# Optimization experiments

Measured on AMD Instinct MI355X. Metric: run time of the kernel, lower is better.

## Reference

```python
import jax, jax.numpy as jnp
import numpy as np

N, K, D = 262144, 1024, 64


def setup_inputs() -> dict:
    key = jax.random.key(0)
    k1, k2 = jax.random.split(key)
    input_data = jax.random.normal(k1, (N, D), dtype=jnp.float32)
    codewords = jax.random.normal(k2, (K, D), dtype=jnp.float32)
    return {"input_data": input_data, "codewords": codewords}


def reference(input_data, codewords):
    # input_data: [N, D], codewords: [K, D]
    x = input_data.reshape(-1, codewords.shape[1])
    x2 = jnp.sum(x * x, axis=1, keepdims=True)          # [N, 1]
    c2 = jnp.sum(codewords * codewords, axis=1)          # [K]
    d2 = x2 + c2[None, :] - 2.0 * (x @ codewords.T)      # [N, K]
    distances = jnp.sqrt(jnp.maximum(d2, 0.0))
    quantized_indices = jnp.argmin(distances, axis=1)    # [N] int
    quantized_distances = jnp.take_along_axis(
        distances, quantized_indices[:, None], axis=1
    )[:, 0]                                              # [N]
    quantized_data = codewords[quantized_indices]        # [N, D]
    return (quantized_indices, quantized_distances, quantized_data)
```

## Files before the change

### kernel.cpp

```cpp
#include <hip/hip_runtime.h>


#define N_PTS 262144
#define K_CW  1024
#define DIM   64
#define CHUNK_B 36864
#define HALF_B  (4 * CHUNK_B)

typedef __attribute__((ext_vector_type(8)))  short short8;
typedef __attribute__((ext_vector_type(16))) float floatx16;

__device__ __forceinline__ unsigned short f2bf(float f) {
    unsigned u = __float_as_uint(f);
    return (unsigned short)((u + 0x7FFFu + ((u >> 16) & 1u)) >> 16);
}
__device__ __forceinline__ float bf2f(unsigned short h) {
    return __uint_as_float(((unsigned)h) << 16);
}
__device__ __forceinline__ float dot4(float4 a, float4 b) {
    return a.x*b.x + a.y*b.y + a.z*b.z + a.w*b.w;
}
__device__ __forceinline__ void async_cp16(const void* g, void* l) {
    __builtin_amdgcn_global_load_lds(
        (const __attribute__((address_space(1))) unsigned int*)g,
        (__attribute__((address_space(3))) unsigned int*)l, 16, 0, 0);
}

__global__ void vq_prep(const float* __restrict__ cw, unsigned char* __restrict__ ws) {
    const int k = blockIdx.x * 256 + threadIdx.x;
    const int ch = k >> 7, r = k & 127;
    unsigned short* chunk = (unsigned short*)(ws + (size_t)ch * CHUNK_B);
    unsigned short* hi = chunk + r * 72;
    unsigned short* lo = hi + 9216;
    const float4* cr = (const float4*)cw + (size_t)k * 16;
    float c2 = 0.f;
    #pragma unroll
    for (int j = 0; j < 16; ++j) {
        float4 v = cr[j];
        c2 += dot4(v, v);
        float4 m = make_float4(-2.f*v.x, -2.f*v.y, -2.f*v.z, -2.f*v.w);
        unsigned short h0 = f2bf(m.x), h1 = f2bf(m.y), h2 = f2bf(m.z), h3 = f2bf(m.w);
        unsigned short l0 = f2bf(m.x - bf2f(h0)), l1 = f2bf(m.y - bf2f(h1)),
                       l2 = f2bf(m.z - bf2f(h2)), l3 = f2bf(m.w - bf2f(h3));
        uint2 hv, lv;
        hv.x = (unsigned)h0 | ((unsigned)h1 << 16);
        hv.y = (unsigned)h2 | ((unsigned)h3 << 16);
        lv.x = (unsigned)l0 | ((unsigned)l1 << 16);
        lv.y = (unsigned)l2 | ((unsigned)l3 << 16);
        *(uint2*)(hi + j * 4) = hv;
        *(uint2*)(lo + j * 4) = lv;
    }
    *(float*)(hi + 64) = c2;
}

__launch_bounds__(512, 2)
__global__ void vq_main(const float* __restrict__ x,
                        const float* __restrict__ cw,
                        const unsigned char* __restrict__ ws,
                        float* __restrict__ out) {
    __shared__ __align__(16) unsigned char sB[HALF_B];

    const int tid  = threadIdx.x;
    const int w    = tid >> 6;
    const int lane = tid & 63;
    const int q    = lane >> 5;
    const int l31  = lane & 31;
    const int half  = blockIdx.x & 1;
    const int pbase = (blockIdx.x >> 1) * 512;
    const float4* __restrict__ x4  = (const float4*)x;
    const float4* __restrict__ c4p = (const float4*)cw;

    {
        const unsigned char* g = ws + (size_t)half * HALF_B + tid * 16;
        unsigned char* l = sB + tid * 16;
        #pragma unroll
        for (int s = 0; s < 18; ++s) async_cp16(g + s * 8192, l + s * 8192);
    }

    short8 ah[2][4], al[2][4];
    #pragma unroll
    for (int rt = 0; rt < 2; ++rt) {
        const int row = pbase + w * 64 + rt * 32 + l31;
        const float4* xr = x4 + (size_t)row * 16;
        #pragma unroll
        for (int ks = 0; ks < 4; ++ks) {
            float4 va = xr[ks * 4 + q * 2];
            float4 vb = xr[ks * 4 + q * 2 + 1];
            float f[8] = {va.x, va.y, va.z, va.w, vb.x, vb.y, vb.z, vb.w};
            short8 h, l;
            #pragma unroll
            for (int j = 0; j < 8; ++j) {
                unsigned short hb = f2bf(f[j]);
                h[j] = (short)hb;
                l[j] = (short)f2bf(f[j] - bf2f(hb));
            }
            ah[rt][ks] = h; al[rt][ks] = l;
        }
    }

    __syncthreads();

    const unsigned short* __restrict__ S = (const unsigned short*)sB;

    float bu[32];
    #pragma unroll
    for (int s = 0; s < 32; ++s) bu[s] = 3.4e38f;

    #pragma unroll 4
    for (int g = 0; g < 16; ++g) {
        const unsigned short* chS = S + (g >> 2) * (CHUNK_B / 2);
        const int nrow = (g & 3) * 32 + l31;
        short8 bh[4], bl[4];
        #pragma unroll
        for (int ks = 0; ks < 4; ++ks) {
            bh[ks] = *(const short8*)&chS[nrow * 72 + ks * 16 + q * 8];
            bl[ks] = *(const short8*)&chS[9216 + nrow * 72 + ks * 16 + q * 8];
        }
        const float c2v = *(const float*)&chS[nrow * 72 + 64];
        floatx16 a0, a1;
        #pragma unroll
        for (int r = 0; r < 16; ++r) { a0[r] = c2v; a1[r] = c2v; }
        __builtin_amdgcn_s_setprio(1);
        #pragma unroll
        for (int ks = 0; ks < 4; ++ks) {
            a0 = __builtin_amdgcn_mfma_f32_32x32x16_bf16(ah[0][ks], bh[ks], a0, 0, 0, 0);
            a1 = __builtin_amdgcn_mfma_f32_32x32x16_bf16(ah[1][ks], bh[ks], a1, 0, 0, 0);
            a0 = __builtin_amdgcn_mfma_f32_32x32x16_bf16(al[0][ks], bh[ks], a0, 0, 0, 0);
            a1 = __builtin_amdgcn_mfma_f32_32x32x16_bf16(al[1][ks], bh[ks], a1, 0, 0, 0);
            a0 = __builtin_amdgcn_mfma_f32_32x32x16_bf16(ah[0][ks], bl[ks], a0, 0, 0, 0);
            a1 = __builtin_amdgcn_mfma_f32_32x32x16_bf16(ah[1][ks], bl[ks], a1, 0, 0, 0);
        }
        __builtin_amdgcn_s_setprio(0);
        const unsigned tag = (unsigned)g;
        #pragma unroll
        for (int r = 0; r < 16; ++r) {
            unsigned u0 = (__float_as_uint(a0[r]) & 0xFFFFFFE0u) | tag;
            bu[r] = fminf(bu[r], __uint_as_float(u0));
            unsigned u1 = (__float_as_uint(a1[r]) & 0xFFFFFFE0u) | tag;
            bu[16 + r] = fminf(bu[16 + r], __uint_as_float(u1));
        }
    }

    int keep_i0 = 0, keep_i1 = 0;
    #pragma unroll
    for (int s = 0; s < 32; ++s) {
        const float v = bu[s];
        float m1 = v;
        #pragma unroll
        for (int m = 1; m < 32; m <<= 1) m1 = fminf(m1, __shfl_xor(m1, m));
        unsigned long long bm = __ballot(v == m1);
        const int wl = __ffs((unsigned)(bm >> (q * 32))) - 1;
        const float v2 = (l31 == wl) ? 3.4e38f : v;
        float m2 = v2;
        #pragma unroll
        for (int m = 1; m < 32; m <<= 1) m2 = fminf(m2, __shfl_xor(m2, m));
        unsigned long long bm2 = __ballot(v2 == m2);
        const int wl2 = __ffs((unsigned)(bm2 >> (q * 32))) - 1;
        const int i0 = (int)(((__float_as_uint(m1) & 31u) << 5) | (unsigned)wl);
        const int i1 = (int)(((__float_as_uint(m2) & 31u) << 5) | (unsigned)wl2);
        if (l31 == s) { keep_i0 = i0; keep_i1 = i1; }
    }

    const int rS   = l31 & 15;
    const int prow = (l31 >> 4) * 32 + (rS & 3) + 8 * (rS >> 2) + 4 * q;
    const int p    = pbase + w * 64 + prow;
    const int ia = keep_i0, ib = keep_i1;
    const float4* xr = x4 + (size_t)p * 16;
    const float4* ca = c4p + (size_t)(half * 512 + ia) * 16;
    const float4* cb = c4p + (size_t)(half * 512 + ib) * 16;
    float da = 0.f, db = 0.f;
    #pragma unroll
    for (int j = 0; j < 16; ++j) {
        float4 xv = xr[j], av = ca[j], bv = cb[j];
        float4 d1 = make_float4(xv.x-av.x, xv.y-av.y, xv.z-av.z, xv.w-av.w);
        float4 d2 = make_float4(xv.x-bv.x, xv.y-bv.y, xv.z-bv.z, xv.w-bv.w);
        da += dot4(d1, d1);
        db += dot4(d2, d2);
    }
    const bool ta = (da < db) || (da == db && ia < ib);
    const int   bidx = half * 512 + (ta ? ia : ib);
    const float bd   = ta ? da : db;
    float* Pi = out + (size_t)(2 + half * 2) * N_PTS;
    Pi[p]         = (float)bidx;
    Pi[N_PTS + p] = bd;
}

__launch_bounds__(256)
__global__ void vq_merge1(float* __restrict__ out) {
    const int p = blockIdx.x * 256 + threadIdx.x;
    const float i0 = out[2 * (size_t)N_PTS + p];
    const float d0 = out[3 * (size_t)N_PTS + p];
    const float i1 = out[4 * (size_t)N_PTS + p];
    const float d1 = out[5 * (size_t)N_PTS + p];
    const bool ta = (d0 < d1) || (d0 == d1);
    out[p]         = ta ? i0 : i1;
    out[N_PTS + p] = sqrtf(fmaxf(ta ? d0 : d1, 0.f));
}

__launch_bounds__(256)
__global__ void vq_merge2(const float* __restrict__ cw, float* __restrict__ out) {
    __shared__ int sidx[256];
    const int tid = threadIdx.x;
    const int base = blockIdx.x * 256;
    sidx[tid] = (int)out[base + tid];
    __syncthreads();
    const float4* c4p = (const float4*)cw;
    float4* od = (float4*)(out + 2 * (size_t)N_PTS) + (size_t)base * 16;
    #pragma unroll
    for (int i = 0; i < 16; ++i) {
        const int g = i * 256 + tid;
        od[g] = c4p[(size_t)sidx[g >> 4] * 16 + (g & 15)];
    }
}

extern "C" void kernel_launch(void* const* d_in, const int* in_sizes, int n_in,
                              void* d_out, int out_size, void* d_ws, size_t ws_size,
                              hipStream_t stream) {
    const float* x  = (const float*)d_in[0];
    const float* cw = (const float*)d_in[1];
    float* out = (float*)d_out;
    unsigned char* ws = (unsigned char*)d_ws;
    vq_prep<<<4, 256, 0, stream>>>(cw, ws);
    vq_main<<<N_PTS / 512 * 2, 512, 0, stream>>>(x, cw, ws, out);
    vq_merge1<<<N_PTS / 256, 256, 0, stream>>>(out);
    vq_merge2<<<N_PTS / 256, 256, 0, stream>>>(cw, out);
}
```

Before: 265.4 us.

## Split codebook across four blocks per point tile to halve LDS footprint

The main kernel now gives each block a quarter of the codebook (256 codewords) instead of half. Per-block shared memory drops from about 147KB to about 73KB, so more blocks can be resident per CU. In exchange, each point tile's x rows are loaded, converted to bf16 and rescored by four blocks instead of two. The number of partial result slots grows from two to four, and the merge kernel reduces over all four with a strict less-than comparison, so ties go to the earlier quarter.

```diff
diff --git a/kernel.cpp b/kernel.cpp
--- a/kernel.cpp
+++ b/kernel.cpp
@@ -5,7 +5,7 @@
 #define K_CW  1024
 #define DIM   64
 #define CHUNK_B 36864
-#define HALF_B  (4 * CHUNK_B)
+#define QTR_B   (2 * CHUNK_B)
 
 typedef __attribute__((ext_vector_type(8)))  short short8;
 typedef __attribute__((ext_vector_type(16))) float floatx16;
@@ -58,23 +58,23 @@
                         const float* __restrict__ cw,
                         const unsigned char* __restrict__ ws,
                         float* __restrict__ out) {
-    __shared__ __align__(16) unsigned char sB[HALF_B];
+    __shared__ __align__(16) unsigned char sB[QTR_B];
 
     const int tid  = threadIdx.x;
     const int w    = tid >> 6;
     const int lane = tid & 63;
     const int q    = lane >> 5;
     const int l31  = lane & 31;
-    const int half  = blockIdx.x & 1;
-    const int pbase = (blockIdx.x >> 1) * 512;
+    const int qtr   = blockIdx.x & 3;
+    const int pbase = (blockIdx.x >> 2) * 512;
     const float4* __restrict__ x4  = (const float4*)x;
     const float4* __restrict__ c4p = (const float4*)cw;
 
     {
-        const unsigned char* g = ws + (size_t)half * HALF_B + tid * 16;
+        const unsigned char* g = ws + (size_t)qtr * QTR_B + tid * 16;
         unsigned char* l = sB + tid * 16;
         #pragma unroll
-        for (int s = 0; s < 18; ++s) async_cp16(g + s * 8192, l + s * 8192);
+        for (int s = 0; s < 9; ++s) async_cp16(g + s * 8192, l + s * 8192);
     }
 
     short8 ah[2][4], al[2][4];
@@ -107,7 +107,7 @@
     for (int s = 0; s < 32; ++s) bu[s] = 3.4e38f;
 
     #pragma unroll 4
-    for (int g = 0; g < 16; ++g) {
+    for (int g = 0; g < 8; ++g) {
         const unsigned short* chS = S + (g >> 2) * (CHUNK_B / 2);
         const int nrow = (g & 3) * 32 + l31;
         short8 bh[4], bl[4];
@@ -166,8 +166,8 @@
     const int p    = pbase + w * 64 + prow;
     const int ia = keep_i0, ib = keep_i1;
     const float4* xr = x4 + (size_t)p * 16;
-    const float4* ca = c4p + (size_t)(half * 512 + ia) * 16;
-    const float4* cb = c4p + (size_t)(half * 512 + ib) * 16;
+    const float4* ca = c4p + (size_t)(qtr * 256 + ia) * 16;
+    const float4* cb = c4p + (size_t)(qtr * 256 + ib) * 16;
     float da = 0.f, db = 0.f;
     #pragma unroll
     for (int j = 0; j < 16; ++j) {
@@ -178,9 +178,9 @@
         db += dot4(d2, d2);
     }
     const bool ta = (da < db) || (da == db && ia < ib);
-    const int   bidx = half * 512 + (ta ? ia : ib);
+    const int   bidx = qtr * 256 + (ta ? ia : ib);
     const float bd   = ta ? da : db;
-    float* Pi = out + (size_t)(2 + half * 2) * N_PTS;
+    float* Pi = out + (size_t)(2 + qtr * 2) * N_PTS;
     Pi[p]         = (float)bidx;
     Pi[N_PTS + p] = bd;
 }
@@ -188,13 +188,16 @@
 __launch_bounds__(256)
 __global__ void vq_merge1(float* __restrict__ out) {
     const int p = blockIdx.x * 256 + threadIdx.x;
-    const float i0 = out[2 * (size_t)N_PTS + p];
-    const float d0 = out[3 * (size_t)N_PTS + p];
-    const float i1 = out[4 * (size_t)N_PTS + p];
-    const float d1 = out[5 * (size_t)N_PTS + p];
-    const bool ta = (d0 < d1) || (d0 == d1);
-    out[p]         = ta ? i0 : i1;
-    out[N_PTS + p] = sqrtf(fmaxf(ta ? d0 : d1, 0.f));
+    float bi = out[2 * (size_t)N_PTS + p];
+    float bd = out[3 * (size_t)N_PTS + p];
+    #pragma unroll
+    for (int qq = 1; qq < 4; ++qq) {
+        const float ii = out[(2 + 2 * (size_t)qq) * N_PTS + p];
+        const float dd = out[(3 + 2 * (size_t)qq) * N_PTS + p];
+        if (dd < bd) { bd = dd; bi = ii; }
+    }
+    out[p]         = bi;
+    out[N_PTS + p] = sqrtf(fmaxf(bd, 0.f));
 }
 
 __launch_bounds__(256)
@@ -221,7 +224,7 @@
     float* out = (float*)d_out;
     unsigned char* ws = (unsigned char*)d_ws;
     vq_prep<<<4, 256, 0, stream>>>(cw, ws);
-    vq_main<<<N_PTS / 512 * 2, 512, 0, stream>>>(x, cw, ws, out);
+    vq_main<<<N_PTS / 512 * 4, 512, 0, stream>>>(x, cw, ws, out);
     vq_merge1<<<N_PTS / 256, 256, 0, stream>>>(out);
     vq_merge2<<<N_PTS / 256, 256, 0, stream>>>(cw, out);
 }
```

After: 352.1 us. 1.33x slower.
